# Performance work log

Hardware: AMD Instinct MI355X
Metric: run time of the kernel (lower is better)

The kernel has to match this reference:

```python
import jax, jax.numpy as jnp
import numpy as np

B, S, D, H = 4, 4096, 1024, 16
DV = D // H


def setup_inputs() -> dict:
    key = jax.random.key(0)
    ks = jax.random.split(key, 8)
    def gl(k, shape):  # glorot-uniform-ish init
        fan_in, fan_out = shape[0], shape[-1]
        lim = np.sqrt(6.0 / (fan_in + fan_out)).astype(np.float32)
        return jax.random.uniform(k, shape, jnp.float32, -lim, lim)
    return {
        "q": jax.random.normal(ks[0], (B, S, D), jnp.float32),
        "k": jax.random.normal(ks[1], (B, S, D), jnp.float32),
        "v": jax.random.normal(ks[2], (B, S, D), jnp.float32),
        "wq": gl(ks[3], (D, H)), "bq": jnp.zeros((H,), jnp.float32),
        "wk": gl(ks[4], (D, H)), "bk": jnp.zeros((H,), jnp.float32),
        "wv": gl(ks[5], (D, D)), "bv": jnp.zeros((D,), jnp.float32),
        "wo": gl(ks[6], (D, D)), "bo": jnp.zeros((D,), jnp.float32),
    }


def reference(q, k, v, wq, bq, wk, bk, wv, bv, wo, bo):
    b, s, d = q.shape
    h = wq.shape[1]
    dv = d // h
    # per-head scalar queries/keys, sigmoid feature map phi
    qh = jax.nn.sigmoid(q @ wq + bq)                 # (B,S,H)
    kh = jax.nn.sigmoid(k @ wk + bk)                 # (B,S,H)
    vh = (v @ wv + bv).reshape(b, s, h, dv)          # (B,S,H,DV)
    # phi(k)^T @ v contracts seq -> per-head summary (B,H,DV)
    kv = jnp.einsum("bsh,bshd->bhd", kh, vh)
    # NOTE: original tf code cumsums over axis=1 of (B,H,1,DV): the HEAD axis
    state = jnp.cumsum(kv, axis=1)                   # (B,H,DV)
    # phi(q) @ state, broadcast over seq
    out_h = jnp.einsum("bsh,bhd->bshd", qh, state)   # (B,S,H,DV)
    concat = out_h.reshape(b, s, d)
    return concat @ wo + bo                          # (B,S,D)
```

## Files before the change

### kernel.cpp

```cpp
#include <hip/hip_runtime.h>

#define SS 4096
#define DD 1024
#define HH 16

typedef float nfloat4 __attribute__((ext_vector_type(4)));
typedef __attribute__((ext_vector_type(8))) short bf16x8;
typedef __attribute__((ext_vector_type(4))) float f32x4;

__device__ __forceinline__ short f2bf(float f) {
  union { float f; unsigned u; } z; z.f = f;
  return (short)((z.u + 0x8000u) >> 16);
}

__global__ __launch_bounds__(256) void k_wfrag(
    const float* __restrict__ wq, const float* __restrict__ wk,
    short* __restrict__ wf)
{
  const int m = blockIdx.x;
  const float* __restrict__ w = m ? wk : wq;
  short* __restrict__ dst = wf + m * 16384;
  for (int p = threadIdx.x; p < 2048; p += 256) {
    const int t = p >> 6, l = p & 63;
    const int kbase = t*32 + ((l >> 4) * 8), col = l & 15;
    short v[8];
#pragma unroll
    for (int e = 0; e < 8; ++e)
      v[e] = f2bf(w[(size_t)(kbase + e)*HH + col]);
    short* o = dst + (size_t)p * 8;
#pragma unroll
    for (int e = 0; e < 8; ++e) o[e] = v[e];
  }
}

__global__ __launch_bounds__(256, 2) void k_kh(
    const float* __restrict__ k, const short* __restrict__ wf,
    const float* __restrict__ bk, float* __restrict__ kh,
    float* __restrict__ ksp)
{
  const int t = threadIdx.x;
  const int wid = t >> 6, lane = t & 63;
  const int s0 = blockIdx.x * 16;
  const short* __restrict__ wfm = wf + 16384;

  __shared__ float smem[16 * 1028];

  const short* __restrict__ wfw = wfm + (size_t)(wid*8*64 + lane) * 8;
  bf16x8 afrag[8];
#pragma unroll
  for (int tt = 0; tt < 8; ++tt)
    afrag[tt] = *(const bf16x8*)(wfw + (size_t)(tt*64) * 8);

  {
    const int r0 = wid * 4;
#pragma unroll
    for (int rr = 0; rr < 4; ++rr) {
      const int row = r0 + rr;
      const float* gsrc = k + (size_t)(s0 + row)*DD + lane*4;
      float* lbase = smem + row*1028;
#pragma unroll
      for (int qd = 0; qd < 4; ++qd) {
        __builtin_amdgcn_global_load_lds(
            (const __attribute__((address_space(1))) void*)(gsrc + qd*256),
            (__attribute__((address_space(3))) void*)(lbase + qd*256),
            16, 0, 0);
      }
    }
  }
  __syncthreads();

  const int row = lane & 15, g = lane >> 4;
  const float* __restrict__ xrow = smem + row*1028 + wid*256 + g*8;
  f32x4 acc = {0.f, 0.f, 0.f, 0.f};
#pragma unroll
  for (int tt = 0; tt < 8; ++tt) {
    const float4 lo = *(const float4*)(xrow + tt*32);
    const float4 hi = *(const float4*)(xrow + tt*32 + 4);
    bf16x8 bb;
    bb[0]=f2bf(lo.x); bb[1]=f2bf(lo.y); bb[2]=f2bf(lo.z); bb[3]=f2bf(lo.w);
    bb[4]=f2bf(hi.x); bb[5]=f2bf(hi.y); bb[6]=f2bf(hi.z); bb[7]=f2bf(hi.w);
    acc = __builtin_amdgcn_mfma_f32_16x16x32_bf16(afrag[tt], bb, acc, 0, 0, 0);
  }
  __syncthreads();
  float* red = smem;
  *(f32x4*)&red[(wid*64 + lane)*4] = acc;
  __syncthreads();
  const int orow = t >> 4, ohead = t & 15;
  const int lane2 = ((ohead >> 2) << 4) + orow;
  const int j = ohead & 3;
  const float sacc = red[0*256 + lane2*4 + j] + red[1*256 + lane2*4 + j]
                   + red[2*256 + lane2*4 + j] + red[3*256 + lane2*4 + j];
  const float sig = 1.f/(1.f + __expf(-(sacc + bk[ohead])));
  kh[(size_t)(s0 + orow)*HH + ohead] = sig;
  __syncthreads();
  smem[t] = sig;
  __syncthreads();
  if (t < 16) {
    float s = 0.f;
#pragma unroll
    for (int r = 0; r < 16; ++r) s += smem[r*16 + t];
    ksp[blockIdx.x*16 + t] = s;
  }
}

__global__ __launch_bounds__(256, 8) void k_kvt(
    const float* __restrict__ v, const float* __restrict__ kh,
    float* __restrict__ part)
{
  const int schunk = blockIdx.x;
  const int dchunk = blockIdx.y;
  const int b = blockIdx.z;
  const int t = threadIdx.x;
  const int c = t & 31;
  const int hh2 = (t >> 5) & 1;
  const int g = t >> 6;
  const int d0 = dchunk*128 + c*4;
  float acc[8][4];
#pragma unroll
  for (int h = 0; h < 8; ++h) {
    acc[h][0] = 0.f; acc[h][1] = 0.f; acc[h][2] = 0.f; acc[h][3] = 0.f;
  }
#pragma unroll 2
  for (int jj = 0; jj < 32; ++jj) {
    const int s = (jj*4 + g)*32 + schunk;
    const size_t rb = (size_t)(b*SS + s);
    const float4 v4 = *(const float4*)(v + rb*DD + d0);
    const float4* khp = (const float4*)(kh + rb*HH) + hh2*2;
    const float4 k0 = khp[0], k1 = khp[1];
    const float kk[8] = {k0.x,k0.y,k0.z,k0.w, k1.x,k1.y,k1.z,k1.w};
#pragma unroll
    for (int h = 0; h < 8; ++h) {
      acc[h][0] = fmaf(kk[h], v4.x, acc[h][0]);
      acc[h][1] = fmaf(kk[h], v4.y, acc[h][1]);
      acc[h][2] = fmaf(kk[h], v4.z, acc[h][2]);
      acc[h][3] = fmaf(kk[h], v4.w, acc[h][3]);
    }
  }
  __shared__ float lds[4][2][128];
  const size_t pbase = (size_t)((b*8 + dchunk)*32 + schunk) * 2048;
#pragma unroll
  for (int h = 0; h < 8; ++h) {
    *(float4*)&lds[g][hh2][c*4] =
        make_float4(acc[h][0], acc[h][1], acc[h][2], acc[h][3]);
    __syncthreads();
    {
      const int hh2r = t >> 7, dl = t & 127;
      const float sum = lds[0][hh2r][dl] + lds[1][hh2r][dl]
                      + lds[2][hh2r][dl] + lds[3][hh2r][dl];
      part[pbase + (hh2r*8 + h)*128 + dl] = sum;
    }
    __syncthreads();
  }
}

__global__ __launch_bounds__(256, 8) void k_red(
    const float* __restrict__ part, float* __restrict__ kvt)
{
  const int dchunk = blockIdx.x;
  const int b = blockIdx.y;
  const int hq = blockIdx.z;
  const int t = threadIdx.x;
  const size_t pb = (size_t)((b*8 + dchunk)*32) * 2048;
#pragma unroll
  for (int ho = 0; ho < 2; ++ho) {
    const int h = hq*4 + ho*2 + (t >> 7), dl = t & 127;
    float s = 0.f;
#pragma unroll 8
    for (int sc = 0; sc < 32; ++sc)
      s += part[pb + (size_t)sc*2048 + h*128 + dl];
    kvt[(size_t)(b*16 + h)*1024 + dchunk*128 + dl] = s;
  }
}

__global__ __launch_bounds__(256, 4) void k_kv(
    const float* __restrict__ kvt, const float* __restrict__ wv,
    float* __restrict__ kvp)
{
  const int h = blockIdx.x;
  const int b = blockIdx.y;
  const int dq = blockIdx.z;
  const int t = threadIdx.x;
  const int w = t >> 6, lane = t & 63;
  __shared__ float kvs[256];
  __shared__ float red[256];
  kvs[t] = kvt[(size_t)(b*16 + h)*1024 + dq*256 + t];
  __syncthreads();
  const float* __restrict__ wp = wv + (size_t)(dq*256 + w*64)*DD + h*64 + lane;
  float acc = 0.f;
#pragma unroll 16
  for (int i = 0; i < 64; ++i)
    acc = fmaf(kvs[w*64 + i], wp[(size_t)i*DD], acc);
  red[t] = acc;
  __syncthreads();
  if (t < 64)
    kvp[((size_t)(b*16 + h)*4 + dq)*64 + t] =
        red[t] + red[64+t] + red[128+t] + red[192+t];
}

__global__ __launch_bounds__(256) void k_kvfin(
    const float* __restrict__ kvp, const float* __restrict__ ksp,
    const float* __restrict__ bv, float* __restrict__ kv)
{
  const int b = blockIdx.x;
  const int t = threadIdx.x;
  __shared__ float red[256];
  __shared__ float ksum[16];
  float s = 0.f;
#pragma unroll
  for (int m = 0; m < 16; ++m)
    s += ksp[b*4096 + m*256 + t];
  red[t] = s;
  __syncthreads();
  if (t < 16) {
    float ks = 0.f;
#pragma unroll
    for (int g = 0; g < 16; ++g) ks += red[g*16 + t];
    ksum[t] = ks;
  }
  __syncthreads();
#pragma unroll
  for (int j = 0; j < 4; ++j) {
    const int idx = j*256 + t;
    const int h = idx >> 6;
    const float* kp = kvp + (size_t)(b*16 + h)*256 + (idx & 63);
    kv[(size_t)b*1024 + idx] =
        kp[0] + kp[64] + kp[128] + kp[192] + ksum[h]*bv[idx];
  }
}

__global__ __launch_bounds__(256) void k_w2(
    const float* __restrict__ kv, const float* __restrict__ wo,
    float* __restrict__ W2)
{
  const int bh = blockIdx.x;
  const int b = bh >> 4, h = bh & 15;
  const int t = threadIdx.x;
  __shared__ float st[64];
  if (t < 64) {
    float s = 0.f;
    for (int hp = 0; hp <= h; ++hp) s += kv[(size_t)b*1024 + hp*64 + t];
    st[t] = s;
  }
  __syncthreads();
  const int d0 = t * 4;
  float4 acc = {0.f, 0.f, 0.f, 0.f};
#pragma unroll 4
  for (int dv = 0; dv < 64; ++dv) {
    const float sv = st[dv];
    const float4 w4 = *(const float4*)(wo + (size_t)(h*64 + dv)*DD + d0);
    acc.x = fmaf(sv, w4.x, acc.x);
    acc.y = fmaf(sv, w4.y, acc.y);
    acc.z = fmaf(sv, w4.z, acc.z);
    acc.w = fmaf(sv, w4.w, acc.w);
  }
  *(float4*)(W2 + (size_t)(b*HH + h)*DD + d0) = acc;
}

__global__ __launch_bounds__(256, 2) void k_qout(
    const float* __restrict__ q, const short* __restrict__ wf,
    const float* __restrict__ bq, const float* __restrict__ W2,
    const float* __restrict__ bo, float* __restrict__ out)
{
  const int t = threadIdx.x;
  const int wid = t >> 6, lane = t & 63;
  const int tile = blockIdx.x;
  const int b = tile >> 8;
  const int s0 = tile * 16;

  __shared__ float smem[16 * 1028];

  float4 w2[16];
  {
    const float* w2p = W2 + (size_t)(b*HH)*DD + t*4;
#pragma unroll
    for (int h = 0; h < 16; ++h) w2[h] = *(const float4*)(w2p + h*DD);
  }
  const float4 bo4 = *(const float4*)(bo + t*4);

  const short* __restrict__ wfw = wf + (size_t)(wid*8*64 + lane) * 8;
  bf16x8 afrag[8];
#pragma unroll
  for (int tt = 0; tt < 8; ++tt)
    afrag[tt] = *(const bf16x8*)(wfw + (size_t)(tt*64) * 8);

  {
    const int r0 = wid * 4;
#pragma unroll
    for (int rr = 0; rr < 4; ++rr) {
      const int row = r0 + rr;
      const float* gsrc = q + (size_t)(s0 + row)*DD + lane*4;
      float* lbase = smem + row*1028;
#pragma unroll
      for (int qd = 0; qd < 4; ++qd) {
        __builtin_amdgcn_global_load_lds(
            (const __attribute__((address_space(1))) void*)(gsrc + qd*256),
            (__attribute__((address_space(3))) void*)(lbase + qd*256),
            16, 0, 0);
      }
    }
  }
  __syncthreads();

  const int row = lane & 15, g = lane >> 4;
  const float* __restrict__ xrow = smem + row*1028 + wid*256 + g*8;
  f32x4 acc = {0.f, 0.f, 0.f, 0.f};
#pragma unroll
  for (int tt = 0; tt < 8; ++tt) {
    const float4 lo = *(const float4*)(xrow + tt*32);
    const float4 hi = *(const float4*)(xrow + tt*32 + 4);
    bf16x8 bb;
    bb[0]=f2bf(lo.x); bb[1]=f2bf(lo.y); bb[2]=f2bf(lo.z); bb[3]=f2bf(lo.w);
    bb[4]=f2bf(hi.x); bb[5]=f2bf(hi.y); bb[6]=f2bf(hi.z); bb[7]=f2bf(hi.w);
    acc = __builtin_amdgcn_mfma_f32_16x16x32_bf16(afrag[tt], bb, acc, 0, 0, 0);
  }
  __syncthreads();
  float* red = smem;
  *(f32x4*)&red[(wid*64 + lane)*4] = acc;
  __syncthreads();
  {
    const int orow = t >> 4, ohead = t & 15;
    const int lane2 = ((ohead >> 2) << 4) + orow;
    const int j = ohead & 3;
    const float sacc = red[0*256 + lane2*4 + j] + red[1*256 + lane2*4 + j]
                     + red[2*256 + lane2*4 + j] + red[3*256 + lane2*4 + j];
    const float val = sacc + bq[ohead];
    smem[1024 + orow*16 + ohead] = 1.f/(1.f + __expf(-val));
  }
  __syncthreads();

  const float* qs = smem + 1024;
#pragma unroll
  for (int r = 0; r < 16; ++r) {
    float4 o = bo4;
#pragma unroll
    for (int h = 0; h < 16; ++h) {
      const float qv = qs[r*16 + h];
      o.x = fmaf(qv, w2[h].x, o.x);
      o.y = fmaf(qv, w2[h].y, o.y);
      o.z = fmaf(qv, w2[h].z, o.z);
      o.w = fmaf(qv, w2[h].w, o.w);
    }
    nfloat4 ov = { o.x, o.y, o.z, o.w };
    nfloat4* dst = (nfloat4*)(out + (size_t)(s0 + r)*DD + t*4);
    __builtin_nontemporal_store(ov, dst);
  }
}

extern "C" void kernel_launch(void* const* d_in, const int* in_sizes, int n_in,
                              void* d_out, int out_size, void* d_ws, size_t ws_size,
                              hipStream_t stream)
{
  const float* q  = (const float*)d_in[0];
  const float* k  = (const float*)d_in[1];
  const float* v  = (const float*)d_in[2];
  const float* wq = (const float*)d_in[3];
  const float* bq = (const float*)d_in[4];
  const float* wk = (const float*)d_in[5];
  const float* bk = (const float*)d_in[6];
  const float* wv = (const float*)d_in[7];
  const float* bv = (const float*)d_in[8];
  const float* wo = (const float*)d_in[9];
  const float* bo = (const float*)d_in[10];
  float* out = (float*)d_out;
  float* ws  = (float*)d_ws;

  float* kh  = ws;
  float* kvt = ws + 262144;
  float* kvp = ws + 327680;
  float* ksp = ws + 344064;
  float* kv  = ws + 360448;
  float* W2  = ws + 364544;
  short* wf  = (short*)(ws + 430080);
  float* part = out;

  hipLaunchKernelGGL(k_wfrag, dim3(2), dim3(256), 0, stream,
                     wq, wk, wf);
  hipLaunchKernelGGL(k_kh, dim3(1024), dim3(256), 0, stream,
                     k, wf, bk, kh, ksp);
  hipLaunchKernelGGL(k_kvt, dim3(32, 8, 4), dim3(256), 0, stream,
                     v, kh, part);
  hipLaunchKernelGGL(k_red, dim3(8, 4, 4), dim3(256), 0, stream,
                     part, kvt);
  hipLaunchKernelGGL(k_kv, dim3(16, 4, 4), dim3(256), 0, stream,
                     kvt, wv, kvp);
  hipLaunchKernelGGL(k_kvfin, dim3(4), dim3(256), 0, stream,
                     kvp, ksp, bv, kv);
  hipLaunchKernelGGL(k_w2, dim3(64), dim3(256), 0, stream,
                     kv, wo, W2);
  hipLaunchKernelGGL(k_qout, dim3(1024), dim3(256), 0, stream,
                     q, wf, bq, W2, bo, out);
}
```

Baseline: 81.34 us.

## Stage q/k tiles in LDS as swizzled bf16 via register loads to raise occupancy

In the k_kh and k_qout projection kernels, the fp32 global-to-LDS DMA of each 16x1024 tile is replaced by register float4 loads. Each value is converted to bf16 once and written into an XOR-swizzled bf16 LDS buffer, so the MFMA loop reads bf16x8 fragments directly. This halves LDS usage, and launch bounds rise from 2 to 4 blocks per CU to hide memory latency. In k_qout the W2 register load is deferred until after the MFMA phase to lower register pressure, at the cost of exposing that load latency later.

Result: faster. 79.13 us, median of 2 (-2.7%).

```diff
diff --git a/kernel.cpp b/kernel.cpp
--- a/kernel.cpp
+++ b/kernel.cpp
@@ -33,7 +33,7 @@
   }
 }
 
-__global__ __launch_bounds__(256, 2) void k_kh(
+__global__ __launch_bounds__(256, 4) void k_kh(
     const float* __restrict__ k, const short* __restrict__ wf,
     const float* __restrict__ bk, float* __restrict__ kh,
     float* __restrict__ ksp)
@@ -43,46 +43,42 @@
   const int s0 = blockIdx.x * 16;
   const short* __restrict__ wfm = wf + 16384;
 
-  __shared__ float smem[16 * 1028];
-
+  __shared__ short xs[16 * 1024];
+  __shared__ float red[1024];
+
+  float4 f[16];
+  {
+    const float* srow = k + (size_t)s0 * DD + t*4;
+#pragma unroll
+    for (int j = 0; j < 16; ++j)
+      f[j] = *(const float4*)(srow + (size_t)j * DD);
+  }
   const short* __restrict__ wfw = wfm + (size_t)(wid*8*64 + lane) * 8;
   bf16x8 afrag[8];
 #pragma unroll
   for (int tt = 0; tt < 8; ++tt)
     afrag[tt] = *(const bf16x8*)(wfw + (size_t)(tt*64) * 8);
-
-  {
-    const int r0 = wid * 4;
-#pragma unroll
-    for (int rr = 0; rr < 4; ++rr) {
-      const int row = r0 + rr;
-      const float* gsrc = k + (size_t)(s0 + row)*DD + lane*4;
-      float* lbase = smem + row*1028;
-#pragma unroll
-      for (int qd = 0; qd < 4; ++qd) {
-        __builtin_amdgcn_global_load_lds(
-            (const __attribute__((address_space(1))) void*)(gsrc + qd*256),
-            (__attribute__((address_space(3))) void*)(lbase + qd*256),
-            16, 0, 0);
-      }
-    }
+  __builtin_amdgcn_sched_barrier(0);
+
+#pragma unroll
+  for (int j = 0; j < 16; ++j) {
+    short4 b4;
+    b4.x = f2bf(f[j].x); b4.y = f2bf(f[j].y);
+    b4.z = f2bf(f[j].z); b4.w = f2bf(f[j].w);
+    const int colb = (t*8) ^ ((j & 7) << 4);
+    *(short4*)((char*)xs + j*2048 + colb) = b4;
   }
   __syncthreads();
 
   const int row = lane & 15, g = lane >> 4;
-  const float* __restrict__ xrow = smem + row*1028 + wid*256 + g*8;
+  const char* __restrict__ xrow = (const char*)xs + row*2048;
   f32x4 acc = {0.f, 0.f, 0.f, 0.f};
 #pragma unroll
   for (int tt = 0; tt < 8; ++tt) {
-    const float4 lo = *(const float4*)(xrow + tt*32);
-    const float4 hi = *(const float4*)(xrow + tt*32 + 4);
-    bf16x8 bb;
-    bb[0]=f2bf(lo.x); bb[1]=f2bf(lo.y); bb[2]=f2bf(lo.z); bb[3]=f2bf(lo.w);
-    bb[4]=f2bf(hi.x); bb[5]=f2bf(hi.y); bb[6]=f2bf(hi.z); bb[7]=f2bf(hi.w);
+    const int colb = ((wid*256 + tt*32 + g*8) * 2) ^ ((row & 7) << 4);
+    const bf16x8 bb = *(const bf16x8*)(xrow + colb);
     acc = __builtin_amdgcn_mfma_f32_16x16x32_bf16(afrag[tt], bb, acc, 0, 0, 0);
   }
-  __syncthreads();
-  float* red = smem;
   *(f32x4*)&red[(wid*64 + lane)*4] = acc;
   __syncthreads();
   const int orow = t >> 4, ohead = t & 15;
@@ -93,12 +89,12 @@
   const float sig = 1.f/(1.f + __expf(-(sacc + bk[ohead])));
   kh[(size_t)(s0 + orow)*HH + ohead] = sig;
   __syncthreads();
-  smem[t] = sig;
+  red[t] = sig;
   __syncthreads();
   if (t < 16) {
     float s = 0.f;
 #pragma unroll
-    for (int r = 0; r < 16; ++r) s += smem[r*16 + t];
+    for (int r = 0; r < 16; ++r) s += red[r*16 + t];
     ksp[blockIdx.x*16 + t] = s;
   }
 }
@@ -256,7 +252,7 @@
   *(float4*)(W2 + (size_t)(b*HH + h)*DD + d0) = acc;
 }
 
-__global__ __launch_bounds__(256, 2) void k_qout(
+__global__ __launch_bounds__(256, 4) void k_qout(
     const float* __restrict__ q, const short* __restrict__ wf,
     const float* __restrict__ bq, const float* __restrict__ W2,
     const float* __restrict__ bo, float* __restrict__ out)
@@ -267,54 +263,43 @@
   const int b = tile >> 8;
   const int s0 = tile * 16;
 
-  __shared__ float smem[16 * 1028];
-
-  float4 w2[16];
+  __shared__ short xs[16 * 1024];
+  __shared__ float red[1024];
+  __shared__ float qs[256];
+
+  float4 f[16];
   {
-    const float* w2p = W2 + (size_t)(b*HH)*DD + t*4;
-#pragma unroll
-    for (int h = 0; h < 16; ++h) w2[h] = *(const float4*)(w2p + h*DD);
-  }
-  const float4 bo4 = *(const float4*)(bo + t*4);
-
+    const float* srow = q + (size_t)s0 * DD + t*4;
+#pragma unroll
+    for (int j = 0; j < 16; ++j)
+      f[j] = *(const float4*)(srow + (size_t)j * DD);
+  }
   const short* __restrict__ wfw = wf + (size_t)(wid*8*64 + lane) * 8;
   bf16x8 afrag[8];
 #pragma unroll
   for (int tt = 0; tt < 8; ++tt)
     afrag[tt] = *(const bf16x8*)(wfw + (size_t)(tt*64) * 8);
-
-  {
-    const int r0 = wid * 4;
-#pragma unroll
-    for (int rr = 0; rr < 4; ++rr) {
-      const int row = r0 + rr;
-      const float* gsrc = q + (size_t)(s0 + row)*DD + lane*4;
-      float* lbase = smem + row*1028;
-#pragma unroll
-      for (int qd = 0; qd < 4; ++qd) {
-        __builtin_amdgcn_global_load_lds(
-            (const __attribute__((address_space(1))) void*)(gsrc + qd*256),
-            (__attribute__((address_space(3))) void*)(lbase + qd*256),
-            16, 0, 0);
-      }
-    }
+  __builtin_amdgcn_sched_barrier(0);
+
+#pragma unroll
+  for (int j = 0; j < 16; ++j) {
+    short4 b4;
+    b4.x = f2bf(f[j].x); b4.y = f2bf(f[j].y);
+    b4.z = f2bf(f[j].z); b4.w = f2bf(f[j].w);
+    const int colb = (t*8) ^ ((j & 7) << 4);
+    *(short4*)((char*)xs + j*2048 + colb) = b4;
   }
   __syncthreads();
 
   const int row = lane & 15, g = lane >> 4;
-  const float* __restrict__ xrow = smem + row*1028 + wid*256 + g*8;
+  const char* __restrict__ xrow = (const char*)xs + row*2048;
   f32x4 acc = {0.f, 0.f, 0.f, 0.f};
 #pragma unroll
   for (int tt = 0; tt < 8; ++tt) {
-    const float4 lo = *(const float4*)(xrow + tt*32);
-    const float4 hi = *(const float4*)(xrow + tt*32 + 4);
-    bf16x8 bb;
-    bb[0]=f2bf(lo.x); bb[1]=f2bf(lo.y); bb[2]=f2bf(lo.z); bb[3]=f2bf(lo.w);
-    bb[4]=f2bf(hi.x); bb[5]=f2bf(hi.y); bb[6]=f2bf(hi.z); bb[7]=f2bf(hi.w);
+    const int colb = ((wid*256 + tt*32 + g*8) * 2) ^ ((row & 7) << 4);
+    const bf16x8 bb = *(const bf16x8*)(xrow + colb);
     acc = __builtin_amdgcn_mfma_f32_16x16x32_bf16(afrag[tt], bb, acc, 0, 0, 0);
   }
-  __syncthreads();
-  float* red = smem;
   *(f32x4*)&red[(wid*64 + lane)*4] = acc;
   __syncthreads();
   {
@@ -324,11 +309,18 @@
     const float sacc = red[0*256 + lane2*4 + j] + red[1*256 + lane2*4 + j]
                      + red[2*256 + lane2*4 + j] + red[3*256 + lane2*4 + j];
     const float val = sacc + bq[ohead];
-    smem[1024 + orow*16 + ohead] = 1.f/(1.f + __expf(-val));
-  }
-  __syncthreads();
-
-  const float* qs = smem + 1024;
+    qs[orow*16 + ohead] = 1.f/(1.f + __expf(-val));
+  }
+  __syncthreads();
+
+  float4 w2[16];
+  {
+    const float* w2p = W2 + (size_t)(b*HH)*DD + t*4;
+#pragma unroll
+    for (int h = 0; h < 16; ++h) w2[h] = *(const float4*)(w2p + h*DD);
+  }
+  const float4 bo4 = *(const float4*)(bo + t*4);
+
 #pragma unroll
   for (int r = 0; r < 16; ++r) {
     float4 o = bo4;
```
